# Kernel optimization log

Hardware: AMD Instinct MI355X
Metric: run time of the kernel (lower is better)

## Reference

```python
import jax, jax.numpy as jnp
import numpy as np

B, N, D = 4, 1024, 1024
H, DH = 16, 64
N_LAYERS = 3  # len(mlp_dims) - 1 with implicit_mlp_hiddens=(64, 64)
EPS = 1.1920929e-07  # torch.nn.RMSNorm default eps = finfo(float32).eps


def _rope_tables(n, dtype):
    # lucidrains RotaryEmbedding: theta=10000, interleaved freq repeat
    inv_freq = 1.0 / (10000.0 ** (np.arange(0, DH, 2, dtype=np.float64) / DH))
    t = np.arange(n, dtype=np.float64)[:, None] * inv_freq[None, :]  # [n, DH/2]
    t = np.repeat(t, 2, axis=-1)  # [n, DH], freqs interleaved (f0,f0,f1,f1,...)
    return jnp.asarray(np.cos(t), dtype), jnp.asarray(np.sin(t), dtype)


def _rope_rotate(x, cos, sin):
    # x: [b,h,n,d]; rotate_half on interleaved pairs: (x1,x2) -> (-x2,x1)
    xp = x.reshape(*x.shape[:-1], DH // 2, 2)
    xr = jnp.stack((-xp[..., 1], xp[..., 0]), axis=-1).reshape(x.shape)
    return x * cos + xr * sin


def _attend(q, k, v):
    # rotate_queries_with_cached_keys with no cache: same positions for q and k
    n = q.shape[-2]
    cos, sin = _rope_tables(n, q.dtype)
    q = _rope_rotate(q, cos, sin)
    k = _rope_rotate(k, cos, sin)
    scale = DH ** -0.5
    scores = jnp.einsum('bhqd,bhkd->bhqk', q, k) * scale
    causal = jnp.tril(jnp.ones((n, n), dtype=bool))
    scores = jnp.where(causal, scores, -jnp.inf)
    attn = jax.nn.softmax(scores, axis=-1)
    return jnp.einsum('bhqk,bhkd->bhqd', attn, v)


def _split_heads(x):
    b, n, _ = x.shape
    return x.reshape(b, n, H, DH).transpose(0, 2, 1, 3)  # b h n d


def setup_inputs() -> dict:
    key = jax.random.key(0)
    ks = jax.random.split(key, 6)
    s = 0.02
    return {
        'tokens': jax.random.normal(ks[0], (B, N, D), jnp.float32),
        'gamma': jnp.ones((D,), jnp.float32),                                  # RMSNorm weight
        'Wq': jax.random.normal(ks[1], (D, H * DH), jnp.float32) * s,           # to_queries
        'Wk': jax.random.normal(ks[2], (N_LAYERS, D, H * DH), jnp.float32) * s, # stacked key projections
        'Wv': jax.random.normal(ks[3], (N_LAYERS, D, H * DH), jnp.float32) * s, # stacked value projections
        'Wo': jax.random.normal(ks[4], (H * DH, D), jnp.float32) * s,           # to_out
    }


def reference(tokens, gamma, Wq, Wk, Wv, Wo):
    b, n, d = tokens.shape
    # RMSNorm (prenorm)
    x = tokens * jax.lax.rsqrt(jnp.mean(tokens * tokens, axis=-1, keepdims=True) + EPS) * gamma
    out = _split_heads(x @ Wq)  # queries, [b h n d]
    for i in range(N_LAYERS):
        k = _split_heads(x @ Wk[i])
        v = _split_heads(x @ Wv[i])
        out = _attend(out, k, v)
        if i < N_LAYERS - 1:
            out = jax.nn.silu(out)  # implicit MLP activation between attention stages
    out = out.transpose(0, 2, 1, 3).reshape(b, n, H * DH)  # merge heads
    return out @ Wo
```

## Files before the change

kernel.cpp:

```cpp
#include <hip/hip_runtime.h>


typedef unsigned short u16;
typedef short s16x8 __attribute__((ext_vector_type(8)));
typedef u16 u16x4 __attribute__((ext_vector_type(4)));
typedef float f32x4 __attribute__((ext_vector_type(4)));

typedef __attribute__((address_space(1))) const unsigned int as1c_uint;
typedef __attribute__((address_space(3))) unsigned int as3_uint;

__device__ __forceinline__ float b2f(u16 h) {
  union { unsigned int u; float f; } v; v.u = ((unsigned int)h) << 16; return v.f;
}
__device__ __forceinline__ u16 f2b(float f) {
  union { float f; unsigned int u; } v; v.f = f;
  return (u16)((v.u + 0x7FFFu + ((v.u >> 16) & 1u)) >> 16);
}
__device__ __forceinline__ void gload16(const u16* g, const u16* lds) {
  __builtin_amdgcn_global_load_lds((as1c_uint*)(size_t)g,
                                   (as3_uint*)(unsigned int)(size_t)lds, 16, 0, 0);
}

__global__ __launch_bounds__(256)
void prep_kernel(const float* __restrict__ T, const float* __restrict__ gamma,
                 u16* __restrict__ X, float* __restrict__ ct,
                 float* __restrict__ st, const float* __restrict__ Wq,
                 const float* __restrict__ Wk, const float* __restrict__ Wv,
                 const float* __restrict__ Wo, u16* __restrict__ wt) {
  __shared__ float shbuf[64 * 65];
  const int bid = blockIdx.x, tid = threadIdx.x;
  if (bid < 4096) {
    const int row = bid;
    const float4 v = ((const float4*)(T + (size_t)row * 1024))[tid];
    float ss = v.x * v.x + v.y * v.y + v.z * v.z + v.w * v.w;
#pragma unroll
    for (int msk = 1; msk <= 32; msk <<= 1) ss += __shfl_xor(ss, msk, 64);
    if ((tid & 63) == 0) shbuf[tid >> 6] = ss;
    __syncthreads();
    const float tot = shbuf[0] + shbuf[1] + shbuf[2] + shbuf[3];
    const float r = rsqrtf(tot * (1.0f / 1024.0f) + 1.1920929e-07f);
    const float4 gm = ((const float4*)gamma)[tid];
    u16x4 o;
    o[0] = f2b(v.x * r * gm.x); o[1] = f2b(v.y * r * gm.y);
    o[2] = f2b(v.z * r * gm.z); o[3] = f2b(v.w * r * gm.w);
    *(u16x4*)(X + (size_t)row * 1024 + tid * 4) = o;
  } else if (bid < 4224) {
    const int idx = (bid - 4096) * 256 + tid;
    const int n = idx >> 5, j = idx & 31;
    const double freq = pow(10000.0, -(double)j / 32.0);
    const double a = (double)n * freq;
    ct[idx] = (float)cos(a);
    st[idx] = (float)sin(a);
  } else {
    const int t = bid - 4224;
    const int z = t >> 8, rem = t & 255;
    const float* src = (z == 0) ? Wq
                     : (z <= 3) ? (Wk + (size_t)(z - 1) * 1048576)
                     : (z <= 6) ? (Wv + (size_t)(z - 4) * 1048576)
                                : Wo;
    u16* dst = wt + (size_t)z * 1048576;
    const int bx = (rem & 15) * 64;
    const int by = (rem >> 4) * 64;
    const int tcol = (tid & 15) * 4, trow = tid >> 4;
#pragma unroll
    for (int i = 0; i < 4; ++i) {
      const int r = trow + i * 16;
      const float4 v = *(const float4*)(src + (size_t)(bx + r) * 1024 + by + tcol);
      shbuf[r * 65 + tcol] = v.x; shbuf[r * 65 + tcol + 1] = v.y;
      shbuf[r * 65 + tcol + 2] = v.z; shbuf[r * 65 + tcol + 3] = v.w;
    }
    __syncthreads();
    const int k4 = (tid & 15) * 4;
#pragma unroll
    for (int j2 = 0; j2 < 4; ++j2) {
      const int R = (tid >> 4) + j2 * 16;
      u16x4 o;
      o[0] = f2b(shbuf[k4 * 65 + R]);       o[1] = f2b(shbuf[(k4 + 1) * 65 + R]);
      o[2] = f2b(shbuf[(k4 + 2) * 65 + R]); o[3] = f2b(shbuf[(k4 + 3) * 65 + R]);
      *(u16x4*)&dst[(size_t)(by + R) * 1024 + bx + k4] = o;
    }
  }
}

template <int KIND>
__global__ __launch_bounds__(256, 2)
void gemm_kernel(const u16* __restrict__ A, const u16* __restrict__ Bt,
                 void* __restrict__ Cout, const float* __restrict__ ct,
                 const float* __restrict__ st) {
  constexpr int MB = (KIND == 0) ? 8 : 4;
  constexpr int BM = MB * 32;
  constexpr int ASLOT = BM * 32;
  constexpr int SLOT = (BM + 128) * 32;
  const int p = blockIdx.x;
  const int role = (p & 7) * (KIND == 0 ? 112 : 64) + (p >> 3);
  const int z = (KIND == 0) ? (role >> 7) : (role >> 8);
  const int rem = (KIND == 0) ? (role & 127) : (role & 255);
  const int m0 = (rem >> 3) * BM;
  const int n0 = (rem & 7) * 128;

  const int tid = threadIdx.x;
  const int w = tid >> 6, l = tid & 63;
  const int g = l >> 4, ll = l & 15;
  const int wr = w >> 1, wc = w & 1;

  const u16* Ab;
  const u16* Bb;
  if (KIND == 0) {
    Ab = A + (size_t)m0 * 1024;
    Bb = Bt + (size_t)z * 1048576 + (size_t)n0 * 1024;
  } else {
    Ab = A + (size_t)m0 * 1024 + z * 512;
    Bb = Bt + (size_t)n0 * 1024 + z * 512;
  }

  __shared__ u16 SH[3][SLOT];

  const f32x4 zero = {0.f, 0.f, 0.f, 0.f};
  f32x4 acc[MB][4];
#pragma unroll
  for (int i = 0; i < MB; ++i)
#pragma unroll
    for (int j = 0; j < 4; ++j) acc[i][j] = zero;

  auto stage = [&](int t2) {
    const int slot = t2 % 3;
    const int k0 = t2 * 32;
    const int rsub = l >> 2, sl = l & 3;
#pragma unroll
    for (int c = 0; c < MB / 2; ++c) {
      const int chunk = c * 4 + w;
      const int row = chunk * 16 + rsub;
      const int kk = k0 + ((sl ^ ((row >> 1) & 3)) << 3);
      gload16(Ab + (size_t)row * 1024 + kk, &SH[slot][chunk * 512]);
    }
#pragma unroll
    for (int c = 0; c < 2; ++c) {
      const int chunk = c * 4 + w;
      const int row = chunk * 16 + rsub;
      const int kk = k0 + ((sl ^ ((row >> 1) & 3)) << 3);
      gload16(Bb + (size_t)row * 1024 + kk, &SH[slot][ASLOT + chunk * 512]);
    }
  };

  const int NT = (KIND == 1) ? 16 : 32;
  stage(0); stage(1);

#pragma unroll
  for (int t = 0; t < NT; ++t) {
    if (t < NT - 1) {
      if constexpr (KIND == 0) asm volatile("s_waitcnt vmcnt(6)" ::: "memory");
      else                     asm volatile("s_waitcnt vmcnt(4)" ::: "memory");
    } else {
      asm volatile("s_waitcnt vmcnt(0)" ::: "memory");
    }
    __builtin_amdgcn_s_barrier();

    const int slot = t % 3;
    const u16* As = &SH[slot][0];
    const u16* Bs = &SH[slot][ASLOT];
    s16x8 bfr[4];
#pragma unroll
    for (int nf = 0; nf < 4; ++nf) {
      const int row = wc * 64 + nf * 16 + ll;
      bfr[nf] = *(const s16x8*)&Bs[row * 32 + ((g ^ ((row >> 1) & 3)) << 3)];
    }
    s16x8 af[MB];
#pragma unroll
    for (int mf = 0; mf < MB; ++mf) {
      const int row = wr * (MB * 16) + mf * 16 + ll;
      af[mf] = *(const s16x8*)&As[row * 32 + ((g ^ ((row >> 1) & 3)) << 3)];
    }

    if (t + 2 < NT) stage(t + 2);

    __builtin_amdgcn_s_setprio(1);
#pragma unroll
    for (int mf = 0; mf < MB; ++mf)
#pragma unroll
      for (int nf = 0; nf < 4; ++nf)
        acc[mf][nf] = __builtin_amdgcn_mfma_f32_16x16x32_bf16(af[mf], bfr[nf],
                                                              acc[mf][nf], 0, 0, 0);
    __builtin_amdgcn_s_setprio(0);
  }
  __syncthreads();

  if (KIND == 0) {
    u16* C = (u16*)Cout + (size_t)z * 4194304;
    if (z < 4) {
      const bool doRope = (z >= 1);
      u16* T = &SH[0][0];
#pragma unroll
      for (int mf = 0; mf < MB; ++mf)
#pragma unroll
        for (int nf = 0; nf < 4; ++nf) {
          const int c = wc * 64 + nf * 16 + ll;
#pragma unroll
          for (int rg = 0; rg < 4; ++rg) {
            const int r = wr * (MB * 16) + mf * 16 + g * 4 + rg;
            T[r * 128 + (c ^ ((r & 7) << 4))] = f2b(acc[mf][nf][rg]);
          }
        }
      __syncthreads();
#pragma unroll
      for (int i = 0; i < BM / 16; ++i) {
        const int R = (tid >> 4) + i * 16;
        const int c0 = (tid & 15) * 8;
        s16x8 v = *(const s16x8*)&T[R * 128 + (c0 ^ ((R & 7) << 4))];
        if (doRope) {
          const int n = (m0 + R) & 1023;
          const int j0 = (c0 & 63) >> 1;
          const float4 c4 = *(const float4*)(ct + n * 32 + j0);
          const float4 s4 = *(const float4*)(st + n * 32 + j0);
          s16x8 vo;
#pragma unroll
          for (int pp = 0; pp < 4; ++pp) {
            const float c = ((const float*)&c4)[pp];
            const float s = ((const float*)&s4)[pp];
            const float x0 = b2f((u16)v[2 * pp]), x1 = b2f((u16)v[2 * pp + 1]);
            vo[2 * pp]     = (short)f2b(x0 * c - x1 * s);
            vo[2 * pp + 1] = (short)f2b(x1 * c + x0 * s);
          }
          v = vo;
        }
        *(s16x8*)&C[(size_t)(m0 + R) * 1024 + n0 + c0] = v;
      }
    } else {
#pragma unroll
      for (int mf = 0; mf < MB; ++mf)
#pragma unroll
        for (int nf = 0; nf < 4; ++nf) {
          const int col = n0 + wc * 64 + nf * 16 + ll;
          const int hh = col >> 6, d = col & 63;
          const int mb = m0 + wr * (MB * 16) + mf * 16 + g * 4;
          const int bb = mb >> 10, n = mb & 1023;
          u16x4 pk;
#pragma unroll
          for (int rg = 0; rg < 4; ++rg) pk[rg] = f2b(acc[mf][nf][rg]);
          *(u16x4*)&C[((size_t)((bb * 16 + hh) * 64 + d)) * 1024 + n] = pk;
        }
    }
  } else {
    float* C = (float*)Cout + (size_t)z * 4194304;
#pragma unroll
    for (int mf = 0; mf < MB; ++mf)
#pragma unroll
      for (int nf = 0; nf < 4; ++nf) {
        const int col = n0 + wc * 64 + nf * 16 + ll;
#pragma unroll
        for (int rg = 0; rg < 4; ++rg) {
          const int m = m0 + wr * (MB * 16) + mf * 16 + g * 4 + rg;
          C[(size_t)m * 1024 + col] = acc[mf][nf][rg];
        }
      }
  }
}

__global__ __launch_bounds__(256)
void reduce_kernel(const float* __restrict__ P, float* __restrict__ out) {
  const int i = (blockIdx.x * 256 + threadIdx.x) * 4;
  const float4 a = *(const float4*)(P + i);
  const float4 b = *(const float4*)(P + 4194304 + i);
  float4 o;
  o.x = a.x + b.x; o.y = a.y + b.y; o.z = a.z + b.z; o.w = a.w + b.w;
  *(float4*)(out + i) = o;
}

template <int SILU>
__global__ __launch_bounds__(256)
void attn_kernel(const u16* __restrict__ Q, const u16* __restrict__ K,
                 const u16* __restrict__ Vt, u16* __restrict__ O,
                 const float* __restrict__ ct, const float* __restrict__ st) {
  const int lin = blockIdx.x + (blockIdx.y << 3);
  const int role = (lin & 7) * 64 + (lin >> 3);
  const int p = role & 7, bh = role >> 3;
  const int q_lo = p, q_hi = 15 - p;
  const int b = bh >> 4, h = bh & 15;
  const int tid = threadIdx.x, w = tid >> 6, l = tid & 63;
  const int g = l >> 4, ll = l & 15;

  const u16* Qb = Q + (size_t)(b * 1024) * 1024 + h * 64;
  const u16* Kb = K + (size_t)(b * 1024) * 1024 + h * 64;
  const u16* Vb = Vt + (size_t)((b * 16 + h) * 64) * 1024;
  u16* Ob = O + (size_t)(b * 1024) * 1024 + h * 64;

  __shared__ u16 Ksh[2][128 * 72];
  __shared__ u16 Psh[4][16 * 72];

  s16x8 qfL[2], qfH[2];
  auto loadQ = [&](int qt, s16x8* qf) {
    const int qrow = qt * 64 + w * 16 + ll;
#pragma unroll
    for (int kc = 0; kc < 2; ++kc) {
      const int d0 = kc * 32 + g * 8;
      const int j0 = d0 >> 1;
      const float4 c4 = *(const float4*)(ct + qrow * 32 + j0);
      const float4 s4v = *(const float4*)(st + qrow * 32 + j0);
      const s16x8 qin = *(const s16x8*)(Qb + (size_t)qrow * 1024 + d0);
      s16x8 qo;
#pragma unroll
      for (int pp = 0; pp < 4; ++pp) {
        const float c = ((const float*)&c4)[pp], s = ((const float*)&s4v)[pp];
        const float x0 = b2f((u16)qin[2 * pp]), x1 = b2f((u16)qin[2 * pp + 1]);
        qo[2 * pp]     = (short)f2b((x0 * c - x1 * s) * 0.125f);
        qo[2 * pp + 1] = (short)f2b((x1 * c + x0 * s) * 0.125f);
      }
      qf[kc] = qo;
    }
  };
  loadQ(q_lo, qfL);
  loadQ(q_hi, qfH);

  float lsL[4], lsH[4];
  f32x4 oL[4], oH[4];
  const f32x4 zero = {0.f, 0.f, 0.f, 0.f};
#pragma unroll
  for (int rg = 0; rg < 4; ++rg) { lsL[rg] = 0.f; lsH[rg] = 0.f; }
#pragma unroll
  for (int df = 0; df < 4; ++df) { oL[df] = zero; oH[df] = zero; }

  const int srow = tid >> 2;
  const int sc0 = (tid & 3) * 16;

  s16x8 kr0, kr1, kr2, kr3;
  auto kload = [&](int tt) {
    const u16* kp = Kb + (size_t)(tt * 128 + srow) * 1024 + sc0;
    kr0 = *(const s16x8*)kp;
    kr1 = *(const s16x8*)(kp + 8);
    const u16* kp2 = kp + (size_t)64 * 1024;
    kr2 = *(const s16x8*)kp2;
    kr3 = *(const s16x8*)(kp2 + 8);
  };
  auto kstore = [&](int bf) {
    *(s16x8*)&Ksh[bf][srow * 72 + sc0] = kr0;
    *(s16x8*)&Ksh[bf][srow * 72 + sc0 + 8] = kr1;
    *(s16x8*)&Ksh[bf][(64 + srow) * 72 + sc0] = kr2;
    *(s16x8*)&Ksh[bf][(64 + srow) * 72 + sc0 + 8] = kr3;
  };

  kload(0);
  kstore(0);
  __syncthreads();
  int buf = 0;

  const int iters = (q_hi + 2) >> 1;
  for (int tt = 0; tt < iters; ++tt) {
    const bool pre = (tt + 1 < iters);
    if (pre) kload(tt + 1);

    s16x8 vb[2][2][4];
#pragma unroll
    for (int sub = 0; sub < 2; ++sub)
#pragma unroll
      for (int kc = 0; kc < 2; ++kc)
#pragma unroll
        for (int df = 0; df < 4; ++df)
          vb[sub][kc][df] = *(const s16x8*)(Vb + (size_t)(df * 16 + ll) * 1024 +
                                           (tt * 2 + sub) * 64 + kc * 32 + g * 8);

    auto process = [&](const s16x8* qf, float* ls, f32x4* o, int sub,
                       bool diag) {
      const int rb = sub * 64;
      f32x4 s4[4];
#pragma unroll
      for (int nf = 0; nf < 4; ++nf) {
        const s16x8 kb0 = *(const s16x8*)&Ksh[buf][(rb + nf * 16 + ll) * 72 + g * 8];
        const s16x8 kb1 = *(const s16x8*)&Ksh[buf][(rb + nf * 16 + ll) * 72 + 32 + g * 8];
        f32x4 sv = zero;
        sv = __builtin_amdgcn_mfma_f32_16x16x32_bf16(qf[0], kb0, sv, 0, 0, 0);
        sv = __builtin_amdgcn_mfma_f32_16x16x32_bf16(qf[1], kb1, sv, 0, 0, 0);
        s4[nf] = sv;
      }

      if (diag) {
#pragma unroll
        for (int nf = 0; nf < 4; ++nf)
#pragma unroll
          for (int rg = 0; rg < 4; ++rg)
            if (nf * 16 + ll > w * 16 + g * 4 + rg) s4[nf][rg] = -3.0e38f;
      }

#pragma unroll
      for (int rg = 0; rg < 4; ++rg) {
        float ps = 0.f;
#pragma unroll
        for (int nf = 0; nf < 4; ++nf) {
          const float pv = __expf(s4[nf][rg] - 12.f);
          s4[nf][rg] = pv;
          ps += pv;
        }
        ls[rg] += ps;
      }

#pragma unroll
      for (int nf = 0; nf < 4; ++nf)
#pragma unroll
        for (int rg = 0; rg < 4; ++rg)
          Psh[w][(g * 4 + rg) * 72 + nf * 16 + ll] = f2b(s4[nf][rg]);

#pragma unroll
      for (int kc = 0; kc < 2; ++kc) {
        const s16x8 pa = *(const s16x8*)&Psh[w][ll * 72 + kc * 32 + g * 8];
#pragma unroll
        for (int df = 0; df < 4; ++df)
          o[df] = __builtin_amdgcn_mfma_f32_16x16x32_bf16(pa, vb[sub][kc][df],
                                                          o[df], 0, 0, 0);
      }
    };

    const int ka = 2 * tt, kb2 = 2 * tt + 1;
    process(qfH, lsH, oH, 0, ka == q_hi);
    if (kb2 <= q_hi) process(qfH, lsH, oH, 1, kb2 == q_hi);
    if (ka <= q_lo) process(qfL, lsL, oL, 0, ka == q_lo);
    if (kb2 <= q_lo) process(qfL, lsL, oL, 1, kb2 == q_lo);

    if (pre) kstore(buf ^ 1);
    __syncthreads();
    buf ^= 1;
  }

  auto finish = [&](float* ls, f32x4* o, int qt) {
#pragma unroll
    for (int rg = 0; rg < 4; ++rg) {
      float v = ls[rg];
      v += __shfl_xor(v, 1, 64);
      v += __shfl_xor(v, 2, 64);
      v += __shfl_xor(v, 4, 64);
      v += __shfl_xor(v, 8, 64);
      ls[rg] = 1.f / v;
    }
#pragma unroll
    for (int df = 0; df < 4; ++df)
#pragma unroll
      for (int rg = 0; rg < 4; ++rg) {
        float val = o[df][rg] * ls[rg];
        if (SILU) val = val / (1.f + __expf(-val));
        Ob[(size_t)(qt * 64 + w * 16 + g * 4 + rg) * 1024 + df * 16 + ll] =
            f2b(val);
      }
  };
  finish(lsH, oH, q_hi);
  finish(lsL, oL, q_lo);
}

extern "C" void kernel_launch(void* const* d_in, const int* in_sizes, int n_in,
                              void* d_out, int out_size, void* d_ws, size_t ws_size,
                              hipStream_t stream) {
  (void)in_sizes; (void)n_in; (void)out_size; (void)ws_size;
  const float* tokens = (const float*)d_in[0];
  const float* gamma  = (const float*)d_in[1];
  const float* Wq     = (const float*)d_in[2];
  const float* Wk     = (const float*)d_in[3];
  const float* Wv     = (const float*)d_in[4];
  const float* Wo     = (const float*)d_in[5];
  float* out = (float*)d_out;

  u16* x    = (u16*)d_ws;
  u16* wt   = x + (size_t)4096 * 1024;
  u16* qkv  = wt + (size_t)8 * 1048576;
  u16* outA = qkv + (size_t)7 * 4194304;
  u16* outB = outA + 4194304;
  float* ct = (float*)(outB + 4194304);
  float* st = ct + 32768;
  float* Pp = (float*)(qkv + 1 * 4194304);

  prep_kernel<<<6272, 256, 0, stream>>>(tokens, gamma, x, ct, st,
                                        Wq, Wk, Wv, Wo, wt);
  gemm_kernel<0><<<896, 256, 0, stream>>>(x, wt, qkv, ct, st);

  const size_t M4 = 4194304;
  attn_kernel<1><<<dim3(8, 64), 256, 0, stream>>>(qkv, qkv + 1 * M4, qkv + 4 * M4,
                                                  outA, ct, st);
  attn_kernel<1><<<dim3(8, 64), 256, 0, stream>>>(outA, qkv + 2 * M4, qkv + 5 * M4,
                                                  outB, ct, st);
  attn_kernel<0><<<dim3(8, 64), 256, 0, stream>>>(outB, qkv + 3 * M4, qkv + 6 * M4,
                                                  outA, ct, st);

  gemm_kernel<1><<<512, 256, 0, stream>>>(outA, wt + (size_t)7 * 1048576,
                                          (void*)Pp, ct, st);
  reduce_kernel<<<4096, 256, 0, stream>>>(Pp, out);
}
```

Baseline: 225.9 us.

## Replace split-K output GEMM with full-K 128x64 tiles, drop reduce kernel

The output projection GEMM used split-K over two halves, wrote partial fp32 results to a workspace and summed them in a separate reduce kernel. It now uses 128x64 tiles over the full K dimension, keeping the same block count and writing straight to the output. This removes the partial-sum traffic and one kernel launch. In exchange each block runs twice as many K iterations with a smaller N tile, which lowers data reuse per block.

After: 218.3 us, median of 2. 1.03x faster.

```diff
diff --git a/kernel.cpp b/kernel.cpp
--- a/kernel.cpp
+++ b/kernel.cpp
@@ -88,39 +88,41 @@
                  void* __restrict__ Cout, const float* __restrict__ ct,
                  const float* __restrict__ st) {
   constexpr int MB = (KIND == 0) ? 8 : 4;
+  constexpr int NB = (KIND == 0) ? 4 : 2;
   constexpr int BM = MB * 32;
+  constexpr int BN = NB * 32;
   constexpr int ASLOT = BM * 32;
-  constexpr int SLOT = (BM + 128) * 32;
+  constexpr int SLOT = (BM + BN) * 32;
   const int p = blockIdx.x;
   const int role = (p & 7) * (KIND == 0 ? 112 : 64) + (p >> 3);
-  const int z = (KIND == 0) ? (role >> 7) : (role >> 8);
-  const int rem = (KIND == 0) ? (role & 127) : (role & 255);
-  const int m0 = (rem >> 3) * BM;
-  const int n0 = (rem & 7) * 128;
+  int z, m0, n0;
+  if (KIND == 0) {
+    z = role >> 7;
+    const int rem = role & 127;
+    m0 = (rem >> 3) * BM;
+    n0 = (rem & 7) * BN;
+  } else {
+    z = 0;
+    m0 = (role >> 4) * BM;
+    n0 = (role & 15) * BN;
+  }
 
   const int tid = threadIdx.x;
   const int w = tid >> 6, l = tid & 63;
   const int g = l >> 4, ll = l & 15;
   const int wr = w >> 1, wc = w & 1;
 
-  const u16* Ab;
-  const u16* Bb;
-  if (KIND == 0) {
-    Ab = A + (size_t)m0 * 1024;
-    Bb = Bt + (size_t)z * 1048576 + (size_t)n0 * 1024;
-  } else {
-    Ab = A + (size_t)m0 * 1024 + z * 512;
-    Bb = Bt + (size_t)n0 * 1024 + z * 512;
-  }
+  const u16* Ab = A + (size_t)m0 * 1024;
+  const u16* Bb = Bt + (size_t)z * 1048576 + (size_t)n0 * 1024;
 
   __shared__ u16 SH[3][SLOT];
 
   const f32x4 zero = {0.f, 0.f, 0.f, 0.f};
-  f32x4 acc[MB][4];
+  f32x4 acc[MB][NB];
 #pragma unroll
   for (int i = 0; i < MB; ++i)
 #pragma unroll
-    for (int j = 0; j < 4; ++j) acc[i][j] = zero;
+    for (int j = 0; j < NB; ++j) acc[i][j] = zero;
 
   auto stage = [&](int t2) {
     const int slot = t2 % 3;
@@ -134,7 +136,7 @@
       gload16(Ab + (size_t)row * 1024 + kk, &SH[slot][chunk * 512]);
     }
 #pragma unroll
-    for (int c = 0; c < 2; ++c) {
+    for (int c = 0; c < BN / 64; ++c) {
       const int chunk = c * 4 + w;
       const int row = chunk * 16 + rsub;
       const int kk = k0 + ((sl ^ ((row >> 1) & 3)) << 3);
@@ -142,14 +144,14 @@
     }
   };
 
-  const int NT = (KIND == 1) ? 16 : 32;
+  const int NT = 32;
   stage(0); stage(1);
 
 #pragma unroll
   for (int t = 0; t < NT; ++t) {
     if (t < NT - 1) {
       if constexpr (KIND == 0) asm volatile("s_waitcnt vmcnt(6)" ::: "memory");
-      else                     asm volatile("s_waitcnt vmcnt(4)" ::: "memory");
+      else                     asm volatile("s_waitcnt vmcnt(3)" ::: "memory");
     } else {
       asm volatile("s_waitcnt vmcnt(0)" ::: "memory");
     }
@@ -158,10 +160,10 @@
     const int slot = t % 3;
     const u16* As = &SH[slot][0];
     const u16* Bs = &SH[slot][ASLOT];
-    s16x8 bfr[4];
-#pragma unroll
-    for (int nf = 0; nf < 4; ++nf) {
-      const int row = wc * 64 + nf * 16 + ll;
+    s16x8 bfr[NB];
+#pragma unroll
+    for (int nf = 0; nf < NB; ++nf) {
+      const int row = wc * (NB * 16) + nf * 16 + ll;
       bfr[nf] = *(const s16x8*)&Bs[row * 32 + ((g ^ ((row >> 1) & 3)) << 3)];
     }
     s16x8 af[MB];
@@ -177,7 +179,7 @@
 #pragma unroll
     for (int mf = 0; mf < MB; ++mf)
 #pragma unroll
-      for (int nf = 0; nf < 4; ++nf)
+      for (int nf = 0; nf < NB; ++nf)
         acc[mf][nf] = __builtin_amdgcn_mfma_f32_16x16x32_bf16(af[mf], bfr[nf],
                                                               acc[mf][nf], 0, 0, 0);
     __builtin_amdgcn_s_setprio(0);
@@ -192,7 +194,7 @@
 #pragma unroll
       for (int mf = 0; mf < MB; ++mf)
 #pragma unroll
-        for (int nf = 0; nf < 4; ++nf) {
+        for (int nf = 0; nf < NB; ++nf) {
           const int c = wc * 64 + nf * 16 + ll;
 #pragma unroll
           for (int rg = 0; rg < 4; ++rg) {
@@ -228,7 +230,7 @@
 #pragma unroll
       for (int mf = 0; mf < MB; ++mf)
 #pragma unroll
-        for (int nf = 0; nf < 4; ++nf) {
+        for (int nf = 0; nf < NB; ++nf) {
           const int col = n0 + wc * 64 + nf * 16 + ll;
           const int hh = col >> 6, d = col & 63;
           const int mb = m0 + wr * (MB * 16) + mf * 16 + g * 4;
@@ -240,12 +242,12 @@
         }
     }
   } else {
-    float* C = (float*)Cout + (size_t)z * 4194304;
+    float* C = (float*)Cout;
 #pragma unroll
     for (int mf = 0; mf < MB; ++mf)
 #pragma unroll
-      for (int nf = 0; nf < 4; ++nf) {
-        const int col = n0 + wc * 64 + nf * 16 + ll;
+      for (int nf = 0; nf < NB; ++nf) {
+        const int col = n0 + wc * (NB * 16) + nf * 16 + ll;
 #pragma unroll
         for (int rg = 0; rg < 4; ++rg) {
           const int m = m0 + wr * (MB * 16) + mf * 16 + g * 4 + rg;
@@ -253,16 +255,6 @@
         }
       }
   }
-}
-
-__global__ __launch_bounds__(256)
-void reduce_kernel(const float* __restrict__ P, float* __restrict__ out) {
-  const int i = (blockIdx.x * 256 + threadIdx.x) * 4;
-  const float4 a = *(const float4*)(P + i);
-  const float4 b = *(const float4*)(P + 4194304 + i);
-  float4 o;
-  o.x = a.x + b.x; o.y = a.y + b.y; o.z = a.z + b.z; o.w = a.w + b.w;
-  *(float4*)(out + i) = o;
 }
 
 template <int SILU>
@@ -461,7 +453,6 @@
   u16* outB = outA + 4194304;
   float* ct = (float*)(outB + 4194304);
   float* st = ct + 32768;
-  float* Pp = (float*)(qkv + 1 * 4194304);
 
   prep_kernel<<<6272, 256, 0, stream>>>(tokens, gamma, x, ct, st,
                                         Wq, Wk, Wv, Wo, wt);
@@ -476,6 +467,5 @@
                                                   outA, ct, st);
 
   gemm_kernel<1><<<512, 256, 0, stream>>>(outA, wt + (size_t)7 * 1048576,
-                                          (void*)Pp, ct, st);
-  reduce_kernel<<<4096, 256, 0, stream>>>(Pp, out);
-}
+                                          (void*)out, ct, st);
+}
```
